# Optimization experiments

Hardware: AMD Instinct MI355X
Metric: run time of the kernel (lower is better)

Reference implementation:

```python
import math
import jax
import jax.numpy as jnp
import numpy as np

N_HE = 50000          # number of hyperedges (molecules)
E = 1200000           # edges per node type (incidence nnz)
IN_FEAT = 200
HE_DIM = 512
E_DIM = 128
Q_DIM = 64
V_DIM = 128
N_M, N_P, N_G = 167, 881, 441   # node counts (fingerprint bit vocabularies)
D_M, D_P, D_G = 167, 881, 441   # node feature dims
SCALE = 1.0 / math.sqrt(Q_DIM)


def _seg_attn(k, q, v, src, dst, n_dst):
    # per-edge score <k[src], q[dst]>/sqrt(q_dim) -> leaky_relu -> softmax over edges sharing dst -> weighted scatter-sum of v[src]
    att = jax.nn.leaky_relu(jnp.sum(k[src] * q[dst], axis=-1) * SCALE)
    m = jax.ops.segment_max(att, dst, num_segments=n_dst)
    m = jnp.where(jnp.isfinite(m), m, 0.0)  # guard empty segments
    ex = jnp.exp(att - m[dst])
    denom = jax.ops.segment_sum(ex, dst, num_segments=n_dst)
    agg = jax.ops.segment_sum(ex[:, None] * v[src], dst, num_segments=n_dst)
    return agg / jnp.maximum(denom, 1e-20)[:, None]


def setup_inputs() -> dict:
    key = jax.random.key(0)
    ks = iter(jax.random.split(key, 64))

    def nrm(shape, scale=1.0):
        return jax.random.normal(next(ks), shape, jnp.float32) * scale

    def lin(din, dout):
        return nrm((din, dout), 1.0 / math.sqrt(din)), jnp.zeros((dout,), jnp.float32)

    inp = {}
    inp["he_feat"] = nrm((N_HE, IN_FEAT))
    inp["maccs_feat"] = nrm((N_M, D_M))
    inp["pubchem_feat"] = nrm((N_P, D_P))
    inp["erg_feat"] = nrm((N_G, D_G))
    inp["w1_w"], inp["w1_b"] = lin(IN_FEAT, HE_DIM)
    inp["w2_w"], inp["w2_b"] = lin(HE_DIM, E_DIM)
    inp["w3_w"], inp["w3_b"] = lin(HE_DIM, Q_DIM)
    inp["w4_w"], inp["w4_b"] = lin(HE_DIM, V_DIM)
    inp["w5m_w"], inp["w5m_b"] = lin(D_M, Q_DIM)
    inp["w5p_w"], inp["w5p_b"] = lin(D_P, Q_DIM)
    inp["w5e_w"], inp["w5e_b"] = lin(D_G, Q_DIM)
    inp["w6m_w"], inp["w6m_b"] = lin(Q_DIM, E_DIM)
    inp["w7m_w"], inp["w7m_b"] = lin(Q_DIM, E_DIM)
    inp["w6p_w"], inp["w6p_b"] = lin(Q_DIM, E_DIM)
    inp["w7p_w"], inp["w7p_b"] = lin(Q_DIM, E_DIM)
    inp["w6e_w"], inp["w6e_b"] = lin(Q_DIM, E_DIM)
    inp["w7e_w"], inp["w7e_b"] = lin(Q_DIM, E_DIM)
    inp["mlp1_w"], inp["mlp1_b"] = lin(3 * E_DIM, 2 * E_DIM)
    inp["mlp2_w"], inp["mlp2_b"] = lin(2 * E_DIM, E_DIM)
    inp["src_maccs"] = jax.random.randint(next(ks), (E,), 0, N_HE, jnp.int32)
    inp["dst_maccs"] = jax.random.randint(next(ks), (E,), 0, N_M, jnp.int32)
    inp["src_pubchem"] = jax.random.randint(next(ks), (E,), 0, N_HE, jnp.int32)
    inp["dst_pubchem"] = jax.random.randint(next(ks), (E,), 0, N_P, jnp.int32)
    inp["src_erg"] = jax.random.randint(next(ks), (E,), 0, N_HE, jnp.int32)
    inp["dst_erg"] = jax.random.randint(next(ks), (E,), 0, N_G, jnp.int32)
    return inp


def reference(he_feat, maccs_feat, pubchem_feat, erg_feat,
              w1_w, w1_b, w2_w, w2_b, w3_w, w3_b, w4_w, w4_b,
              w5m_w, w5m_b, w5p_w, w5p_b, w5e_w, w5e_b,
              w6m_w, w6m_b, w7m_w, w7m_b,
              w6p_w, w6p_b, w7p_w, w7p_b,
              w6e_w, w6e_b, w7e_w, w7e_b,
              mlp1_w, mlp1_b, mlp2_w, mlp2_b,
              src_maccs, dst_maccs, src_pubchem, dst_pubchem, src_erg, dst_erg):
    n_he = he_feat.shape[0]
    e_feat = he_feat @ w1_w + w1_b            # [N_HE, he_dim] (w1, first_layer=True)
    k_he = e_feat @ w3_w + w3_b               # [N_HE, q_dim]
    v_he = e_feat @ w4_w + w4_b               # [N_HE, v_dim]
    q_from_nodes = e_feat @ w2_w + w2_b       # [N_HE, e_dim]
    groups = [
        (maccs_feat, w5m_w, w5m_b, w6m_w, w6m_b, w7m_w, w7m_b, src_maccs, dst_maccs),
        (pubchem_feat, w5p_w, w5p_b, w6p_w, w6p_b, w7p_w, w7p_b, src_pubchem, dst_pubchem),
        (erg_feat, w5e_w, w5e_b, w6e_w, w6e_b, w7e_w, w7e_b, src_erg, dst_erg),
    ]
    msgs = []
    for feat, w5w, w5b, w6w, w6b, w7w, w7b, src, dst in groups:
        q = feat @ w5w + w5b                  # node queries [N_t, q_dim]
        # hyperedge -> node attention (writes node 'feat'; not consumed by this forward's output, kept for fidelity)
        _node_feat_new = _seg_attn(k_he, q, v_he, src, dst, feat.shape[0])
        # node -> hyperedge attention (note: uses q, i.e. the pre-update node projection, as in the source)
        k2 = q @ w6w + w6b                    # [N_t, e_dim]
        v2 = q @ w7w + w7b                    # [N_t, e_dim]
        msgs.append(_seg_attn(k2, q_from_nodes, v2, dst, src, n_he))
    he_new = jnp.concatenate(msgs, axis=-1)   # [N_HE, 3*e_dim]
    x = jax.nn.relu(he_new @ mlp1_w + mlp1_b)  # dropout: eval mode -> identity
    x = jax.nn.relu(x @ mlp2_w + mlp2_b)
    return x                                   # [N_HE, e_dim] (last_layer=False, eval)
```

## Files before the change

### kernel.cpp

```cpp
#include <hip/hip_runtime.h>
#include <hip/hip_bf16.h>

typedef __hip_bfloat16 bf16;
typedef float f32x4 __attribute__((ext_vector_type(4)));
typedef short bf16x8s __attribute__((ext_vector_type(8)));
typedef unsigned short u16x8 __attribute__((ext_vector_type(8)));

constexpr int N_HE = 50000;
constexpr int M_PAD = 50048;
constexpr int E_EDGES = 1200000;
constexpr int IN_F = 200;
constexpr int KP_HE = 224;
constexpr int HE_DIM = 512;
constexpr int E_DIM = 128;
constexpr int Q_DIM = 64;
constexpr float SL2E = 0.125f * 1.44269504088896f;
constexpr int N_NODES = 1489;
constexpr int R_STRIDE = 216;
constexpr int T_STRIDE = 192;
constexpr int LDSD = 40;
constexpr int NBIN = 98;
constexpr int BIN_SHIFT = 9;
constexpr int ECHUNK = 4096;
constexpr int BINCAP = 13056;

struct EdgeIdx { const int* p[3]; };

__device__ __forceinline__ void split2(float v, bf16& h, bf16& l)
{
    bf16 hb = __float2bfloat16(v);
    h = hb;
    l = __float2bfloat16(v - __bfloat162float(hb));
}
__device__ __forceinline__ void split2u(float v, unsigned short& h, unsigned short& l)
{
    bf16 hb = __float2bfloat16(v);
    bf16 lb = __float2bfloat16(v - __bfloat162float(hb));
    h = *reinterpret_cast<unsigned short*>(&hb);
    l = *reinterpret_cast<unsigned short*>(&lb);
}
__device__ __forceinline__ float exp2_fast(float x)
{
    float r;
    asm("v_exp_f32 %0, %1" : "=v"(r) : "v"(x));
    return r;
}

struct PrepArgs {
    const float *w1w, *w1b, *w2w, *w2b;
    float *W12f, *b12;
    const float *w6[3], *b6[3];
    float *Bkvf;
    const float *w7[3], *b7[3];
    const float *mlp1w, *mlp1b;
    bf16 *Wct_hi, *Wct_lo;
    float *b_comp;
    const float *mlp2w;
    bf16 *Wm2t_hi, *Wm2t_lo;
    const float *feat[3], *w5[3], *b5[3];
    float *q_t;
    int *bincursor;
};

__global__ __launch_bounds__(256) void prep_fused_kernel(PrepArgs P)
{
    __shared__ float sh[256];
    int bid = blockIdx.x, tid = threadIdx.x;
    if (bid < 201) {
        int row = bid;
        int col = tid & 127, ks = tid >> 7;
        const float* a = (row < IN_F) ? (P.w1w + (size_t)row * HE_DIM) : P.w1b;
        float s = 0.f;
#pragma unroll 4
        for (int k = ks; k < HE_DIM; k += 2)
            s = fmaf(a[k], P.w2w[k * E_DIM + col], s);
        sh[ks * 128 + col] = s;
        __syncthreads();
        if (ks == 0) {
            float v = sh[col] + sh[128 + col];
            if (row < IN_F) P.W12f[row * E_DIM + col] = v;
            else P.b12[col] = v + P.w2b[col];
        }
    } else if (bid < 329) {
        int k = bid - 201;
        int c = tid;
        if (c < R_STRIDE) {
            int g = c / 72, j = c - g * 72;
            float v = 0.f;
            if (j < 64) v = P.w6[g][j * E_DIM + k];
            else if (j == 64) v = P.b6[g][k];
            P.Bkvf[k * R_STRIDE + c] = v;
        }
    } else if (bid < 522) {
        int row = bid - 329;
        int n = tid;
        if (row < 192) {
            int g = row >> 6, i = row & 63;
            const float* w7 = P.w7[g];
            float s = 0.f;
#pragma unroll 4
            for (int k = 0; k < 128; ++k)
                s = fmaf(w7[i * 128 + k], P.mlp1w[(size_t)(g * 128 + k) * 256 + n], s);
            bf16 h, l; split2(s, h, l);
            P.Wct_hi[n * T_STRIDE + row] = h;
            P.Wct_lo[n * T_STRIDE + row] = l;
        } else {
            float s = P.mlp1b[n];
            for (int g = 0; g < 3; ++g)
#pragma unroll 4
                for (int k = 0; k < 128; ++k)
                    s = fmaf(P.b7[g][k], P.mlp1w[(size_t)(g * 128 + k) * 256 + n], s);
            P.b_comp[n] = s;
        }
    } else if (bid < 650) {
        int n = bid - 522;
        int k = tid;
        float v = P.mlp2w[(size_t)k * 128 + n];
        bf16 h, l; split2(v, h, l);
        P.Wm2t_hi[n * 256 + k] = h;
        P.Wm2t_lo[n * 256 + k] = l;
    } else if (bid < 650 + N_NODES) {
        int b = bid - 650;
        int g = (b < 167) ? 0 : (b < 1048 ? 1 : 2);
        int row = b - (g == 0 ? 0 : (g == 1 ? 167 : 1048));
        int Dt = (g == 0) ? 167 : (g == 1 ? 881 : 441);
        const float* feat = P.feat[g] + (size_t)row * Dt;
        const float* w5 = P.w5[g];
        int col = tid & 63, ks = tid >> 6;
        float s = 0.f;
#pragma unroll 4
        for (int k = ks; k < Dt; k += 4)
            s = fmaf(feat[k], w5[k * Q_DIM + col], s);
        sh[ks * 64 + col] = s;
        __syncthreads();
        if (ks == 0)
            P.q_t[(size_t)b * Q_DIM + col] =
                sh[col] + sh[64 + col] + sh[128 + col] + sh[192 + col] + P.b5[g][col];
    } else {
        int idx = (bid - (650 + N_NODES)) * 256 + tid;
        if (idx < 3 * NBIN) P.bincursor[idx] = 0;
    }
}

__global__ __launch_bounds__(256) void bin_scatter_kernel(
    EdgeIdx S, EdgeIdx D, int* __restrict__ bincursor, unsigned* __restrict__ binbuf)
{
    int g = blockIdx.y;
    const int* src = S.p[g];
    const int* dst = D.p[g];
    __shared__ unsigned stage[ECHUNK];
    __shared__ int hist4[4][NBIN];
    __shared__ int hist[NBIN], off[NBIN], cur[NBIN], gbase[NBIN];
    int tid = threadIdx.x, lane = tid & 63, w = tid >> 6;
    for (int b = tid; b < 4 * NBIN; b += 256) (&hist4[0][0])[b] = 0;
    __syncthreads();

    int base = blockIdx.x * ECHUNK;
    int s[ECHUNK / 256], d[ECHUNK / 256];
#pragma unroll
    for (int k = 0; k < ECHUNK / 256; ++k) {
        int i = base + k * 256 + tid;
        if (i < E_EDGES) {
            s[k] = src[i];
            d[k] = dst[i];
            atomicAdd(&hist4[w][s[k] >> BIN_SHIFT], 1);
        } else s[k] = -1;
    }
    __syncthreads();
    if (w == 0) {
        int i1 = 64 + lane;
        int v0 = 0, v1 = 0;
        if (lane < NBIN) v0 = hist4[0][lane] + hist4[1][lane] + hist4[2][lane] + hist4[3][lane];
        if (i1 < NBIN) v1 = hist4[0][i1] + hist4[1][i1] + hist4[2][i1] + hist4[3][i1];
        int x0 = v0, x1 = v1;
#pragma unroll
        for (int o = 1; o < 64; o <<= 1) {
            int t0 = __shfl_up(x0, o, 64);
            int t1 = __shfl_up(x1, o, 64);
            if (lane >= o) { x0 += t0; x1 += t1; }
        }
        int tot0 = __shfl(x0, 63, 64);
        if (lane < NBIN) { hist[lane] = v0; off[lane] = x0 - v0; cur[lane] = x0 - v0; }
        if (i1 < NBIN) { hist[i1] = v1; off[i1] = tot0 + x1 - v1; cur[i1] = tot0 + x1 - v1; }
    }
    __syncthreads();
    if (tid < NBIN) gbase[tid] = hist[tid] ? atomicAdd(&bincursor[g * NBIN + tid], hist[tid]) : 0;
    __syncthreads();
#pragma unroll
    for (int k = 0; k < ECHUNK / 256; ++k) {
        if (s[k] >= 0) {
            int bin = s[k] >> BIN_SHIFT;
            int pos = atomicAdd(&cur[bin], 1);
            stage[pos] = ((unsigned)(s[k] & 511) << 10) | (unsigned)d[k];
        }
    }
    __syncthreads();
    size_t gslot = (size_t)g * NBIN * BINCAP;
    for (int b = w; b < NBIN; b += 4) {
        int len = hist[b];
        if (!len) continue;
        int gb = gbase[b];
        int avail = BINCAP - gb;
        if (avail <= 0) continue;
        if (len > avail) len = avail;
        int lo = off[b];
        size_t obase = gslot + (size_t)b * BINCAP + gb;
        for (int j = lane; j < len; j += 64)
            binbuf[obase + j] = stage[lo + j];
    }
}

__global__ __launch_bounds__(256) void csr_wr_fused_kernel(
    const unsigned* __restrict__ binbuf, const int* __restrict__ bincursor,
    int2* __restrict__ rows2_all, int* __restrict__ ebuf,
    const float* __restrict__ W12f, const float* __restrict__ b12,
    const float* __restrict__ Bkvf,
    bf16* __restrict__ WRt_hi, bf16* __restrict__ WRt_lo, float* __restrict__ bR)
{
    __shared__ int hist[512], cur[512], cs[8];
    __shared__ float fcol[128];
    int bid = blockIdx.x, tid = threadIdx.x;
    if (bid < 3 * NBIN) {
        int g = bid / NBIN, b = bid - g * NBIN;
        int cnt = min(bincursor[g * NBIN + b], BINCAP);
        size_t sbase = ((size_t)g * NBIN + b) * BINCAP;
        int h0 = b << BIN_SHIFT;
        int hN = min(512, N_HE - h0);
        int ebase_rel = b * BINCAP;
        int2* rows2 = rows2_all + g * N_HE;
        int lane = tid & 63, w = tid >> 6;
        hist[tid] = 0; hist[tid + 256] = 0;
        __syncthreads();
        for (int i = tid; i < cnt; i += 256)
            atomicAdd(&hist[binbuf[sbase + i] >> 10], 1);
        __syncthreads();
#pragma unroll
        for (int c2 = 0; c2 < 2; ++c2) {
            int c = w * 2 + c2, idx = c * 64 + lane;
            int v = hist[idx], x = v;
#pragma unroll
            for (int o = 1; o < 64; o <<= 1) {
                int t = __shfl_up(x, o, 64);
                if (lane >= o) x += t;
            }
            cur[idx] = x - v;
            if (lane == 63) cs[c] = x;
        }
        __syncthreads();
        if (tid == 0) {
            int run = 0;
#pragma unroll
            for (int c = 0; c < 8; ++c) { int t = cs[c]; cs[c] = run; run += t; }
        }
        __syncthreads();
#pragma unroll
        for (int c2 = 0; c2 < 2; ++c2) {
            int c = w * 2 + c2, idx = c * 64 + lane;
            int e = cur[idx] + cs[c];
            cur[idx] = e;
            if (idx < hN) rows2[h0 + idx] = make_int2(ebase_rel + e, ebase_rel + e + hist[idx]);
        }
        __syncthreads();
        for (int i = tid; i < cnt; i += 256) {
            unsigned p = binbuf[sbase + i];
            int pos = atomicAdd(&cur[p >> 10], 1);
            ebuf[sbase + pos] = (int)((p & 1023u) << 8);
        }
    } else {
        int c = bid - 3 * NBIN;
        const bf16 z = __float2bfloat16(0.f);
        if (c >= R_STRIDE) {
            if (tid < KP_HE) { WRt_hi[c * KP_HE + tid] = z; WRt_lo[c * KP_HE + tid] = z; }
            return;
        }
        if (tid < 128) fcol[tid] = Bkvf[tid * R_STRIDE + c];
        __syncthreads();
        if (tid < IN_F) {
            const float* wrow = W12f + (size_t)tid * E_DIM;
            float s = 0.f;
#pragma unroll 4
            for (int k = 0; k < 128; ++k) s = fmaf(wrow[k], fcol[k], s);
            bf16 h, l; split2(s * SL2E, h, l);
            WRt_hi[c * KP_HE + tid] = h;
            WRt_lo[c * KP_HE + tid] = l;
        } else if (tid < KP_HE) {
            WRt_hi[c * KP_HE + tid] = z;
            WRt_lo[c * KP_HE + tid] = z;
        } else if (tid == KP_HE) {
            float s = 0.f;
            for (int k = 0; k < 128; ++k) s = fmaf(b12[k], fcol[k], s);
            bR[c] = s * SL2E;
        }
    }
}

template <bool GUARD, bool BIAS, bool RELU>
__global__ __launch_bounds__(256) void mfma_gemm_kernel(
    const float* __restrict__ A, int lda, int Kp, int Mvalid,
    const bf16* __restrict__ Bthg, const bf16* __restrict__ Btlg,
    const float* __restrict__ bias,
    float* __restrict__ C, int M, int N, int ldc)
{
    __shared__ bf16 Ah[128 * LDSD], Al[128 * LDSD], Bh[64 * LDSD], Bl[64 * LDSD];
    const int tid = threadIdx.x;
    const int bm = blockIdx.x * 128, bn = blockIdx.y * 64;
    const int lane = tid & 63, w = tid >> 6;
    const int kgrp = lane >> 4, lr = lane & 15;
    const int arow = tid >> 1, ahalf = (tid & 1) * 16;
    const int brow = tid >> 2, bq = (tid & 3) * 8;
    f32x4 acc[2][4] = {};

    for (int k0 = 0; k0 < Kp; k0 += 32) {
        {
            int row = bm + arow, kb = k0 + ahalf;
            float va[16];
            if (!GUARD || (row < Mvalid && kb + 16 <= lda)) {
                const float* ap = A + (size_t)row * lda + kb;
                *(float4*)&va[0]  = *(const float4*)ap;
                *(float4*)&va[4]  = *(const float4*)(ap + 4);
                *(float4*)&va[8]  = *(const float4*)(ap + 8);
                *(float4*)&va[12] = *(const float4*)(ap + 12);
            } else {
#pragma unroll
                for (int j = 0; j < 16; ++j) {
                    int k = kb + j;
                    va[j] = (row < Mvalid && k < lda) ? A[(size_t)row * lda + k] : 0.f;
                }
            }
            u16x8 H0, H1, L0, L1;
#pragma unroll
            for (int j = 0; j < 8; ++j) {
                unsigned short h, l;
                split2u(va[j], h, l);       H0[j] = h; L0[j] = l;
                split2u(va[8 + j], h, l);   H1[j] = h; L1[j] = l;
            }
            *(u16x8*)&Ah[arow * LDSD + ahalf] = H0;
            *(u16x8*)&Ah[arow * LDSD + ahalf + 8] = H1;
            *(u16x8*)&Al[arow * LDSD + ahalf] = L0;
            *(u16x8*)&Al[arow * LDSD + ahalf + 8] = L1;
            const size_t bbase = (size_t)(bn + brow) * Kp + k0 + bq;
            uint4 w0 = *(const uint4*)(Bthg + bbase);
            uint4 w1 = *(const uint4*)(Btlg + bbase);
            *(uint4*)&Bh[brow * LDSD + bq] = w0;
            *(uint4*)&Bl[brow * LDSD + bq] = w1;
        }
        __syncthreads();
        bf16x8s afh[2], afl[2], bfh[4], bfl[4];
#pragma unroll
        for (int mi = 0; mi < 2; ++mi) {
            int r = w * 32 + mi * 16 + lr;
            afh[mi] = *(const bf16x8s*)&Ah[r * LDSD + kgrp * 8];
            afl[mi] = *(const bf16x8s*)&Al[r * LDSD + kgrp * 8];
        }
#pragma unroll
        for (int ni = 0; ni < 4; ++ni) {
            int r = ni * 16 + lr;
            bfh[ni] = *(const bf16x8s*)&Bh[r * LDSD + kgrp * 8];
            bfl[ni] = *(const bf16x8s*)&Bl[r * LDSD + kgrp * 8];
        }
#pragma unroll
        for (int mi = 0; mi < 2; ++mi)
#pragma unroll
            for (int ni = 0; ni < 4; ++ni) {
                acc[mi][ni] = __builtin_amdgcn_mfma_f32_16x16x32_bf16(afh[mi], bfh[ni], acc[mi][ni], 0, 0, 0);
                acc[mi][ni] = __builtin_amdgcn_mfma_f32_16x16x32_bf16(afl[mi], bfh[ni], acc[mi][ni], 0, 0, 0);
                acc[mi][ni] = __builtin_amdgcn_mfma_f32_16x16x32_bf16(afh[mi], bfl[ni], acc[mi][ni], 0, 0, 0);
            }
        __syncthreads();
    }

#pragma unroll
    for (int mi = 0; mi < 2; ++mi) {
#pragma unroll
        for (int ni = 0; ni < 4; ++ni) {
            int col = bn + ni * 16 + lr;
            float bv = 0.f;
            if (BIAS) bv = (col < N) ? bias[col] : 0.f;
            int row0 = bm + w * 32 + mi * 16 + kgrp * 4;
#pragma unroll
            for (int r = 0; r < 4; ++r) {
                float v = acc[mi][ni][r] + bv;
                if (RELU) v = fmaxf(v, 0.f);
                int row = row0 + r;
                if (row < M && col < N) C[(size_t)row * ldc + col] = v;
            }
        }
    }
}

__global__ __launch_bounds__(256) void attn_kernel(
    const float* __restrict__ R,
    const float* __restrict__ q_t,
    const int2* __restrict__ rows2_all,
    const int* __restrict__ ebuf_all,
    float* __restrict__ T)
{
    int wid = blockIdx.x * 4 + (threadIdx.x >> 6);
    int lane = threadIdx.x & 63;
    int g = wid / N_HE;
    int h = wid - g * N_HE;
    const int toff_tab[3] = {0, 167, 1048};
    const char* qb = (const char*)(q_t + (size_t)toff_tab[g] * Q_DIM);
    const int* ebuf = ebuf_all + (size_t)g * NBIN * BINCAP;
    int2 se = rows2_all[g * N_HE + h];
    int start = se.x, end = se.y;

    int sub = lane >> 4, sl = lane & 15;
    const float* Rrow = R + (size_t)h * R_STRIDE + g * 72;
    float4 r4 = *reinterpret_cast<const float4*>(Rrow + sl * 4);
    float ch = Rrow[64];
    int slo = sl * 16;

    float denom = 0.f;
    float acc0 = 0.f, acc1 = 0.f, acc2 = 0.f, acc3 = 0.f;

    for (int i0 = start + sub * 2; i0 < end; i0 += 8) {
        bool ok1 = (i0 + 1) < end;
        int o0 = ebuf[i0];
        int o1 = ebuf[ok1 ? i0 + 1 : i0];
        float4 t0 = *reinterpret_cast<const float4*>(qb + o0 + slo);
        float4 t1 = *reinterpret_cast<const float4*>(qb + o1 + slo);
        float p0 = t0.x * r4.x;
        p0 = fmaf(t0.y, r4.y, p0); p0 = fmaf(t0.z, r4.z, p0); p0 = fmaf(t0.w, r4.w, p0);
        float p1 = t1.x * r4.x;
        p1 = fmaf(t1.y, r4.y, p1); p1 = fmaf(t1.z, r4.z, p1); p1 = fmaf(t1.w, r4.w, p1);
#pragma unroll
        for (int mask = 1; mask < 16; mask <<= 1) {
            p0 += __shfl_xor(p0, mask, 64);
            p1 += __shfl_xor(p1, mask, 64);
        }
        float s0 = p0 + ch; s0 = fmaxf(s0, 0.01f * s0);
        float s1 = p1 + ch; s1 = fmaxf(s1, 0.01f * s1);
        float w0 = exp2_fast(s0);
        float w1 = ok1 ? exp2_fast(s1) : 0.f;
        denom += w0 + w1;
        acc0 = fmaf(w0, t0.x, fmaf(w1, t1.x, acc0));
        acc1 = fmaf(w0, t0.y, fmaf(w1, t1.y, acc1));
        acc2 = fmaf(w0, t0.z, fmaf(w1, t1.z, acc2));
        acc3 = fmaf(w0, t0.w, fmaf(w1, t1.w, acc3));
    }

    denom += __shfl_xor(denom, 16, 64); denom += __shfl_xor(denom, 32, 64);
    acc0 += __shfl_xor(acc0, 16, 64); acc0 += __shfl_xor(acc0, 32, 64);
    acc1 += __shfl_xor(acc1, 16, 64); acc1 += __shfl_xor(acc1, 32, 64);
    acc2 += __shfl_xor(acc2, 16, 64); acc2 += __shfl_xor(acc2, 32, 64);
    acc3 += __shfl_xor(acc3, 16, 64); acc3 += __shfl_xor(acc3, 32, 64);
    if (sub == 0) {
        float rden = 1.f / fmaxf(denom, 1e-20f);
        float4 o = {acc0 * rden, acc1 * rden, acc2 * rden, acc3 * rden};
        *reinterpret_cast<float4*>(T + (size_t)h * T_STRIDE + g * 64 + sl * 4) = o;
    }
}

extern "C" void kernel_launch(void* const* d_in, const int* in_sizes, int n_in,
                              void* d_out, int out_size, void* d_ws, size_t ws_size,
                              hipStream_t stream)
{
    const float* he_feat = (const float*)d_in[0];
    float* out = (float*)d_out;

    EdgeIdx Esrc, Edst;
    for (int g = 0; g < 3; ++g) {
        Esrc.p[g] = (const int*)d_in[34 + 2 * g];
        Edst.p[g] = (const int*)d_in[35 + 2 * g];
    }

    char* base = (char*)d_ws;
    size_t off = 0;
    auto alloc = [&](size_t bytes) -> void* {
        void* r = (void*)(base + off);
        off = (off + bytes + 255) & ~(size_t)255;
        return r;
    };
    float* W12f = (float*)alloc(IN_F * E_DIM * 4);
    float* b12 = (float*)alloc(E_DIM * 4);
    float* Bkvf = (float*)alloc(E_DIM * R_STRIDE * 4);
    bf16* WRt_hi = (bf16*)alloc(256 * KP_HE * 2);
    bf16* WRt_lo = (bf16*)alloc(256 * KP_HE * 2);
    float* bR = (float*)alloc(R_STRIDE * 4);
    bf16* Wct_hi = (bf16*)alloc(256 * T_STRIDE * 2);
    bf16* Wct_lo = (bf16*)alloc(256 * T_STRIDE * 2);
    float* b_comp = (float*)alloc(256 * 4);
    bf16* Wm2t_hi = (bf16*)alloc(128 * 256 * 2);
    bf16* Wm2t_lo = (bf16*)alloc(128 * 256 * 2);
    float* q_t = (float*)alloc(N_NODES * Q_DIM * 4);
    int* bincursor = (int*)alloc(3 * NBIN * 4);
    int2* rows2 = (int2*)alloc((size_t)3 * N_HE * 8);
    size_t T_start = off;
    float* T = (float*)alloc((size_t)M_PAD * T_STRIDE * 4);
    size_t R_start = off;
    float* R = (float*)alloc((size_t)N_HE * R_STRIDE * 4);
    int* ebuf = (int*)alloc((size_t)3 * NBIN * BINCAP * 4);
    unsigned* binbuf = (unsigned*)(base + T_start);
    float* h1 = (float*)(base + R_start);

    PrepArgs P;
    P.w1w = (const float*)d_in[4]; P.w1b = (const float*)d_in[5];
    P.w2w = (const float*)d_in[6]; P.w2b = (const float*)d_in[7];
    P.W12f = W12f; P.b12 = b12;
    for (int g = 0; g < 3; ++g) {
        P.w6[g] = (const float*)d_in[18 + 4 * g];
        P.b6[g] = (const float*)d_in[19 + 4 * g];
        P.w7[g] = (const float*)d_in[20 + 4 * g];
        P.b7[g] = (const float*)d_in[21 + 4 * g];
        P.feat[g] = (const float*)d_in[1 + g];
        P.w5[g] = (const float*)d_in[12 + 2 * g];
        P.b5[g] = (const float*)d_in[13 + 2 * g];
    }
    P.Bkvf = Bkvf;
    P.mlp1w = (const float*)d_in[30]; P.mlp1b = (const float*)d_in[31];
    P.Wct_hi = Wct_hi; P.Wct_lo = Wct_lo; P.b_comp = b_comp;
    P.mlp2w = (const float*)d_in[32];
    P.Wm2t_hi = Wm2t_hi; P.Wm2t_lo = Wm2t_lo;
    P.q_t = q_t;
    P.bincursor = bincursor;
    prep_fused_kernel<<<650 + N_NODES + 2, 256, 0, stream>>>(P);

    {
        dim3 grid((E_EDGES + ECHUNK - 1) / ECHUNK, 3);
        bin_scatter_kernel<<<grid, 256, 0, stream>>>(Esrc, Edst, bincursor, binbuf);
        csr_wr_fused_kernel<<<3 * NBIN + 256, 256, 0, stream>>>(
            binbuf, bincursor, rows2, ebuf, W12f, b12, Bkvf, WRt_hi, WRt_lo, bR);
    }

    const int MB = M_PAD / 128;
    const float* mlp2b = (const float*)d_in[33];
    mfma_gemm_kernel<true, true, false><<<dim3(MB, 4), 256, 0, stream>>>(
        he_feat, IN_F, KP_HE, N_HE, WRt_hi, WRt_lo, bR, R, N_HE, R_STRIDE, R_STRIDE);
    attn_kernel<<<(3 * N_HE) / 4, 256, 0, stream>>>(R, q_t, rows2, ebuf, T);
    mfma_gemm_kernel<false, true, true><<<dim3(MB, 4), 256, 0, stream>>>(
        T, T_STRIDE, T_STRIDE, M_PAD, Wct_hi, Wct_lo, b_comp, h1, M_PAD, 256, 256);
    mfma_gemm_kernel<false, true, true><<<dim3(MB, 2), 256, 0, stream>>>(
        h1, 256, 256, M_PAD, Wm2t_hi, Wm2t_lo, mlp2b, out, N_HE, E_DIM, E_DIM);
}
```

Baseline: 288.5 us.

## Fuse edge bin-scatter into prep kernel and use DPP reductions in attention

Merges the edge binning scatter kernel and the weight/query prep kernel into one launch, with scatter blocks first and prep blocks after, sharing LDS. The bincursor zeroing moves to a hipMemsetAsync because the scatter now runs in the same launch that used to clear it. This removes one kernel launch and lets the two independent stages overlap on the GPU. In the attention kernel, the 16-lane shuffle reduction is replaced with DPP-based row reductions to cut cross-lane shuffle cost. The memset adds a small API call of its own, and the fused kernel's LDS footprint is the larger scatter staging buffer for every block.

```diff
diff --git a/kernel.cpp b/kernel.cpp
--- a/kernel.cpp
+++ b/kernel.cpp
@@ -22,7 +22,10 @@
 constexpr int NBIN = 98;
 constexpr int BIN_SHIFT = 9;
 constexpr int ECHUNK = 4096;
+constexpr int NCHUNK = (E_EDGES + ECHUNK - 1) / ECHUNK;
 constexpr int BINCAP = 13056;
+constexpr int SCAT_BLKS = 3 * NCHUNK;
+constexpr int PREP_BLKS = 650 + N_NODES;
 
 struct EdgeIdx { const int* p[3]; };
 
@@ -44,6 +47,14 @@
     float r;
     asm("v_exp_f32 %0, %1" : "=v"(r) : "v"(x));
     return r;
+}
+__device__ __forceinline__ float red16(float x)
+{
+    x += __int_as_float(__builtin_amdgcn_update_dpp(0, __float_as_int(x), 0xB1, 0xF, 0xF, true));
+    x += __int_as_float(__builtin_amdgcn_update_dpp(0, __float_as_int(x), 0x4E, 0xF, 0xF, true));
+    x += __int_as_float(__builtin_amdgcn_update_dpp(0, __float_as_int(x), 0x141, 0xF, 0xF, true));
+    x += __int_as_float(__builtin_amdgcn_update_dpp(0, __float_as_int(x), 0x140, 0xF, 0xF, true));
+    return x;
 }
 
 struct PrepArgs {
@@ -59,15 +70,82 @@
     bf16 *Wm2t_hi, *Wm2t_lo;
     const float *feat[3], *w5[3], *b5[3];
     float *q_t;
-    int *bincursor;
 };
 
-__global__ __launch_bounds__(256) void prep_fused_kernel(PrepArgs P)
-{
-    __shared__ float sh[256];
+__global__ __launch_bounds__(256) void scatter_prep_fused_kernel(
+    EdgeIdx S, EdgeIdx D, int* __restrict__ bincursor, unsigned* __restrict__ binbuf,
+    PrepArgs P)
+{
+    __shared__ unsigned stage[ECHUNK];
+    __shared__ int hist4[4][NBIN];
+    __shared__ int hist[NBIN], off[NBIN], cur[NBIN], gbase[NBIN];
     int bid = blockIdx.x, tid = threadIdx.x;
-    if (bid < 201) {
-        int row = bid;
+    if (bid < SCAT_BLKS) {
+        int g = bid / NCHUNK, chunk = bid - g * NCHUNK;
+        const int* src = S.p[g];
+        const int* dst = D.p[g];
+        int lane = tid & 63, w = tid >> 6;
+        for (int b = tid; b < 4 * NBIN; b += 256) (&hist4[0][0])[b] = 0;
+        __syncthreads();
+        int base = chunk * ECHUNK;
+        int s[ECHUNK / 256], d[ECHUNK / 256];
+#pragma unroll
+        for (int k = 0; k < ECHUNK / 256; ++k) {
+            int i = base + k * 256 + tid;
+            if (i < E_EDGES) {
+                s[k] = src[i];
+                d[k] = dst[i];
+                atomicAdd(&hist4[w][s[k] >> BIN_SHIFT], 1);
+            } else s[k] = -1;
+        }
+        __syncthreads();
+        if (w == 0) {
+            int i1 = 64 + lane;
+            int v0 = 0, v1 = 0;
+            if (lane < NBIN) v0 = hist4[0][lane] + hist4[1][lane] + hist4[2][lane] + hist4[3][lane];
+            if (i1 < NBIN) v1 = hist4[0][i1] + hist4[1][i1] + hist4[2][i1] + hist4[3][i1];
+            int x0 = v0, x1 = v1;
+#pragma unroll
+            for (int o = 1; o < 64; o <<= 1) {
+                int t0 = __shfl_up(x0, o, 64);
+                int t1 = __shfl_up(x1, o, 64);
+                if (lane >= o) { x0 += t0; x1 += t1; }
+            }
+            int tot0 = __shfl(x0, 63, 64);
+            if (lane < NBIN) { hist[lane] = v0; off[lane] = x0 - v0; cur[lane] = x0 - v0; }
+            if (i1 < NBIN) { hist[i1] = v1; off[i1] = tot0 + x1 - v1; cur[i1] = tot0 + x1 - v1; }
+        }
+        __syncthreads();
+        if (tid < NBIN) gbase[tid] = hist[tid] ? atomicAdd(&bincursor[g * NBIN + tid], hist[tid]) : 0;
+        __syncthreads();
+#pragma unroll
+        for (int k = 0; k < ECHUNK / 256; ++k) {
+            if (s[k] >= 0) {
+                int bin = s[k] >> BIN_SHIFT;
+                int pos = atomicAdd(&cur[bin], 1);
+                stage[pos] = ((unsigned)(s[k] & 511) << 10) | (unsigned)d[k];
+            }
+        }
+        __syncthreads();
+        size_t gslot = (size_t)g * NBIN * BINCAP;
+        for (int b = w; b < NBIN; b += 4) {
+            int len = hist[b];
+            if (!len) continue;
+            int gb = gbase[b];
+            int avail = BINCAP - gb;
+            if (avail <= 0) continue;
+            if (len > avail) len = avail;
+            int lo = off[b];
+            size_t obase = gslot + (size_t)b * BINCAP + gb;
+            for (int j = lane; j < len; j += 64)
+                binbuf[obase + j] = stage[lo + j];
+        }
+        return;
+    }
+    float* sh = (float*)stage;
+    int pb = bid - SCAT_BLKS;
+    if (pb < 201) {
+        int row = pb;
         int col = tid & 127, ks = tid >> 7;
         const float* a = (row < IN_F) ? (P.w1w + (size_t)row * HE_DIM) : P.w1b;
         float s = 0.f;
@@ -81,8 +159,8 @@
             if (row < IN_F) P.W12f[row * E_DIM + col] = v;
             else P.b12[col] = v + P.w2b[col];
         }
-    } else if (bid < 329) {
-        int k = bid - 201;
+    } else if (pb < 329) {
+        int k = pb - 201;
         int c = tid;
         if (c < R_STRIDE) {
             int g = c / 72, j = c - g * 72;
@@ -91,8 +169,8 @@
             else if (j == 64) v = P.b6[g][k];
             P.Bkvf[k * R_STRIDE + c] = v;
         }
-    } else if (bid < 522) {
-        int row = bid - 329;
+    } else if (pb < 522) {
+        int row = pb - 329;
         int n = tid;
         if (row < 192) {
             int g = row >> 6, i = row & 63;
@@ -112,15 +190,15 @@
                     s = fmaf(P.b7[g][k], P.mlp1w[(size_t)(g * 128 + k) * 256 + n], s);
             P.b_comp[n] = s;
         }
-    } else if (bid < 650) {
-        int n = bid - 522;
+    } else if (pb < 650) {
+        int n = pb - 522;
         int k = tid;
         float v = P.mlp2w[(size_t)k * 128 + n];
         bf16 h, l; split2(v, h, l);
         P.Wm2t_hi[n * 256 + k] = h;
         P.Wm2t_lo[n * 256 + k] = l;
-    } else if (bid < 650 + N_NODES) {
-        int b = bid - 650;
+    } else {
+        int b = pb - 650;
         int g = (b < 167) ? 0 : (b < 1048 ? 1 : 2);
         int row = b - (g == 0 ? 0 : (g == 1 ? 167 : 1048));
         int Dt = (g == 0) ? 167 : (g == 1 ? 881 : 441);
@@ -136,77 +214,6 @@
         if (ks == 0)
             P.q_t[(size_t)b * Q_DIM + col] =
                 sh[col] + sh[64 + col] + sh[128 + col] + sh[192 + col] + P.b5[g][col];
-    } else {
-        int idx = (bid - (650 + N_NODES)) * 256 + tid;
-        if (idx < 3 * NBIN) P.bincursor[idx] = 0;
-    }
-}
-
-__global__ __launch_bounds__(256) void bin_scatter_kernel(
-    EdgeIdx S, EdgeIdx D, int* __restrict__ bincursor, unsigned* __restrict__ binbuf)
-{
-    int g = blockIdx.y;
-    const int* src = S.p[g];
-    const int* dst = D.p[g];
-    __shared__ unsigned stage[ECHUNK];
-    __shared__ int hist4[4][NBIN];
-    __shared__ int hist[NBIN], off[NBIN], cur[NBIN], gbase[NBIN];
-    int tid = threadIdx.x, lane = tid & 63, w = tid >> 6;
-    for (int b = tid; b < 4 * NBIN; b += 256) (&hist4[0][0])[b] = 0;
-    __syncthreads();
-
-    int base = blockIdx.x * ECHUNK;
-    int s[ECHUNK / 256], d[ECHUNK / 256];
-#pragma unroll
-    for (int k = 0; k < ECHUNK / 256; ++k) {
-        int i = base + k * 256 + tid;
-        if (i < E_EDGES) {
-            s[k] = src[i];
-            d[k] = dst[i];
-            atomicAdd(&hist4[w][s[k] >> BIN_SHIFT], 1);
-        } else s[k] = -1;
-    }
-    __syncthreads();
-    if (w == 0) {
-        int i1 = 64 + lane;
-        int v0 = 0, v1 = 0;
-        if (lane < NBIN) v0 = hist4[0][lane] + hist4[1][lane] + hist4[2][lane] + hist4[3][lane];
-        if (i1 < NBIN) v1 = hist4[0][i1] + hist4[1][i1] + hist4[2][i1] + hist4[3][i1];
-        int x0 = v0, x1 = v1;
-#pragma unroll
-        for (int o = 1; o < 64; o <<= 1) {
-            int t0 = __shfl_up(x0, o, 64);
-            int t1 = __shfl_up(x1, o, 64);
-            if (lane >= o) { x0 += t0; x1 += t1; }
-        }
-        int tot0 = __shfl(x0, 63, 64);
-        if (lane < NBIN) { hist[lane] = v0; off[lane] = x0 - v0; cur[lane] = x0 - v0; }
-        if (i1 < NBIN) { hist[i1] = v1; off[i1] = tot0 + x1 - v1; cur[i1] = tot0 + x1 - v1; }
-    }
-    __syncthreads();
-    if (tid < NBIN) gbase[tid] = hist[tid] ? atomicAdd(&bincursor[g * NBIN + tid], hist[tid]) : 0;
-    __syncthreads();
-#pragma unroll
-    for (int k = 0; k < ECHUNK / 256; ++k) {
-        if (s[k] >= 0) {
-            int bin = s[k] >> BIN_SHIFT;
-            int pos = atomicAdd(&cur[bin], 1);
-            stage[pos] = ((unsigned)(s[k] & 511) << 10) | (unsigned)d[k];
-        }
-    }
-    __syncthreads();
-    size_t gslot = (size_t)g * NBIN * BINCAP;
-    for (int b = w; b < NBIN; b += 4) {
-        int len = hist[b];
-        if (!len) continue;
-        int gb = gbase[b];
-        int avail = BINCAP - gb;
-        if (avail <= 0) continue;
-        if (len > avail) len = avail;
-        int lo = off[b];
-        size_t obase = gslot + (size_t)b * BINCAP + gb;
-        for (int j = lane; j < len; j += 64)
-            binbuf[obase + j] = stage[lo + j];
     }
 }
 
@@ -424,11 +431,8 @@
         p0 = fmaf(t0.y, r4.y, p0); p0 = fmaf(t0.z, r4.z, p0); p0 = fmaf(t0.w, r4.w, p0);
         float p1 = t1.x * r4.x;
         p1 = fmaf(t1.y, r4.y, p1); p1 = fmaf(t1.z, r4.z, p1); p1 = fmaf(t1.w, r4.w, p1);
-#pragma unroll
-        for (int mask = 1; mask < 16; mask <<= 1) {
-            p0 += __shfl_xor(p0, mask, 64);
-            p1 += __shfl_xor(p1, mask, 64);
-        }
+        p0 = red16(p0);
+        p1 = red16(p1);
         float s0 = p0 + ch; s0 = fmaxf(s0, 0.01f * s0);
         float s1 = p1 + ch; s1 = fmaxf(s1, 0.01f * s1);
         float w0 = exp2_fast(s0);
@@ -494,6 +498,8 @@
     unsigned* binbuf = (unsigned*)(base + T_start);
     float* h1 = (float*)(base + R_start);
 
+    hipMemsetAsync(bincursor, 0, 3 * NBIN * 4, stream);
+
     PrepArgs P;
     P.w1w = (const float*)d_in[4]; P.w1b = (const float*)d_in[5];
     P.w2w = (const float*)d_in[6]; P.w2b = (const float*)d_in[7];
@@ -513,15 +519,11 @@
     P.mlp2w = (const float*)d_in[32];
     P.Wm2t_hi = Wm2t_hi; P.Wm2t_lo = Wm2t_lo;
     P.q_t = q_t;
-    P.bincursor = bincursor;
-    prep_fused_kernel<<<650 + N_NODES + 2, 256, 0, stream>>>(P);
-
-    {
-        dim3 grid((E_EDGES + ECHUNK - 1) / ECHUNK, 3);
-        bin_scatter_kernel<<<grid, 256, 0, stream>>>(Esrc, Edst, bincursor, binbuf);
-        csr_wr_fused_kernel<<<3 * NBIN + 256, 256, 0, stream>>>(
-            binbuf, bincursor, rows2, ebuf, W12f, b12, Bkvf, WRt_hi, WRt_lo, bR);
-    }
+    scatter_prep_fused_kernel<<<SCAT_BLKS + PREP_BLKS, 256, 0, stream>>>(
+        Esrc, Edst, bincursor, binbuf, P);
+
+    csr_wr_fused_kernel<<<3 * NBIN + 256, 256, 0, stream>>>(
+        binbuf, bincursor, rows2, ebuf, W12f, b12, Bkvf, WRt_hi, WRt_lo, bR);
 
     const int MB = M_PAD / 128;
     const float* mlp2b = (const float*)d_in[33];
```

Result: faster. 278.8 us (-3.4%).
